# Kernel tuning notes

Hardware: AMD Instinct MI355X
Metric: run time of the kernel (lower is better)

The kernel has to match this reference:

```python
import jax, jax.numpy as jnp
import numpy as np

NUM_SAMPLES = 2048
MAX_AGENTS = 64
D_MODEL = 128
NUM_HEADS = 8


def setup_inputs() -> dict:
    key = jax.random.key(0)
    # deterministic ragged sizes: 1..64 repeating -> total = 32 * (64*65/2) = 66560
    agents = ((np.arange(NUM_SAMPLES) % MAX_AGENTS) + 1).astype(np.int32)
    total = int(agents.sum())
    k1, k2, k3 = jax.random.split(key, 3)
    s = 1.0 / np.sqrt(D_MODEL)
    return {
        "att_in": jax.random.normal(k1, (total, D_MODEL), jnp.float32),
        "in_proj_w": jax.random.uniform(k2, (3 * D_MODEL, D_MODEL), jnp.float32, -s, s),
        "in_proj_b": jnp.zeros((3 * D_MODEL,), jnp.float32),
        "out_proj_w": jax.random.uniform(k3, (D_MODEL, D_MODEL), jnp.float32, -s, s),
        "out_proj_b": jnp.zeros((D_MODEL,), jnp.float32),
        "agents_per_sample": jnp.asarray(agents),
    }


def reference(att_in, in_proj_w, in_proj_b, out_proj_w, out_proj_b, agents_per_sample):
    # agents_per_sample is static ragged metadata (host ints)
    agents = np.asarray(agents_per_sample)
    B = len(agents)
    A = int(agents.max())
    D = att_in.shape[-1]
    hd = D // NUM_HEADS

    # scatter ragged tokens into zero-padded [B, A, D]
    sample_ids = np.repeat(np.arange(B), agents)
    pos = np.concatenate([np.arange(n) for n in agents])
    padded = jnp.zeros((B, A, D), att_in.dtype).at[sample_ids, pos].set(att_in)
    key_valid = jnp.asarray(np.arange(A)[None, :] < agents[:, None])  # [B, A]

    # torch nn.MultiheadAttention math (eval mode, dropout=0)
    qkv = padded @ in_proj_w.T + in_proj_b  # [B, A, 3D]
    q, k, v = jnp.split(qkv, 3, axis=-1)
    q = q.reshape(B, A, NUM_HEADS, hd)
    k = k.reshape(B, A, NUM_HEADS, hd)
    v = v.reshape(B, A, NUM_HEADS, hd)

    scores = jnp.einsum("bqhd,bkhd->bhqk", q, k) / jnp.sqrt(jnp.asarray(hd, q.dtype))
    scores = jnp.where(key_valid[:, None, None, :], scores, jnp.asarray(-1e30, scores.dtype))
    attn = jax.nn.softmax(scores, axis=-1)

    out = jnp.einsum("bhqk,bkhd->bqhd", attn, v).reshape(B, A, D)
    out = out @ out_proj_w.T + out_proj_b

    # unpad: concatenation of the per-sample ragged outputs
    return out[sample_ids, pos]
```

## Files before the change

kernel.cpp:

```cpp
#include <hip/hip_runtime.h>

#define DM 128

typedef __attribute__((ext_vector_type(8))) __bf16 bf16x8;
typedef __attribute__((ext_vector_type(4))) float f32x4;

__device__ inline unsigned short f2bf(float f) {
    unsigned u = __float_as_uint(f);
    u += 0x7FFFu + ((u >> 16) & 1u);
    return (unsigned short)(u >> 16);
}

__global__ void prep(const int* __restrict__ agents, int B, int M,
                     const float* __restrict__ wqkv, const float* __restrict__ wout,
                     const float* __restrict__ x,
                     int* __restrict__ offs,
                     unsigned short* __restrict__ wqkv_bf,
                     unsigned short* __restrict__ wout_bf,
                     unsigned short* __restrict__ xbf) {
    if (blockIdx.x < 64) {
        int idx = (blockIdx.x * 256 + threadIdx.x) * 4;
        if (idx < 49152) {
            float4 v = *(const float4*)(wqkv + idx);
            ushort4 o;
            o.x = f2bf(v.x); o.y = f2bf(v.y); o.z = f2bf(v.z); o.w = f2bf(v.w);
            *(ushort4*)(wqkv_bf + idx) = o;
        } else {
            int j = idx - 49152;
            float4 v = *(const float4*)(wout + j);
            ushort4 o;
            o.x = f2bf(v.x); o.y = f2bf(v.y); o.z = f2bf(v.z); o.w = f2bf(v.w);
            *(ushort4*)(wout_bf + j) = o;
        }
    } else if (blockIdx.x == 64) {
        __shared__ int part[256];
        const int tid = threadIdx.x;
        const int per = (B + 255) >> 8;
        const int base = tid * per;
        int s = 0;
        for (int i = 0; i < per; ++i) {
            int idx = base + i;
            if (idx < B) s += agents[idx];
        }
        part[tid] = s;
        __syncthreads();
        for (int off = 1; off < 256; off <<= 1) {
            int v = (tid >= off) ? part[tid - off] : 0;
            __syncthreads();
            part[tid] += v;
            __syncthreads();
        }
        int run = (tid == 0) ? 0 : part[tid - 1];
        for (int i = 0; i < per; ++i) {
            int idx = base + i;
            if (idx < B) { offs[idx] = run; run += agents[idx]; }
        }
    } else {
        const int nf4 = M * 32;
        const int stride = ((int)gridDim.x - 65) * 256;
        for (int idx = ((int)blockIdx.x - 65) * 256 + (int)threadIdx.x; idx < nf4;
             idx += stride) {
            float4 v = ((const float4*)x)[idx];
            ushort4 o;
            o.x = f2bf(v.x); o.y = f2bf(v.y); o.z = f2bf(v.z); o.w = f2bf(v.w);
            ((ushort4*)xbf)[idx] = o;
        }
    }
}

template<int NT>
__device__ __forceinline__ void qa_body(
    const unsigned short* __restrict__ xbf,
    const unsigned short* __restrict__ wqkvb,
    const float* __restrict__ bqkv,
    unsigned short* __restrict__ obuf,
    int n, int base, int M, int h, int quad, int l16)
{
    constexpr int G   = (NT + 1) / 2;
    constexpr int KT2 = 2 * G;
    bf16x8 qf[NT], kf[NT], vA[G];
    #pragma unroll
    for (int g = 0; g < G; ++g) vA[g] = (bf16x8)(__bf16)0.0f;

    bf16x8 wfq[4], wfk[4], wfv[4];
    const unsigned short* wq = wqkvb + (size_t)(h * 16 + l16) * 128;
    #pragma unroll
    for (int ks = 0; ks < 4; ++ks) {
        wfq[ks] = *(const bf16x8*)(wq + ks * 32 + quad * 8);
        wfk[ks] = *(const bf16x8*)(wq + 128 * 128 + ks * 32 + quad * 8);
        wfv[ks] = *(const bf16x8*)(wq + 256 * 128 + ks * 32 + quad * 8);
    }
    const float4 bq4 = *(const float4*)(bqkv + h * 16 + quad * 4);
    const float4 bk4 = *(const float4*)(bqkv + 128 + h * 16 + quad * 4);
    const float  bv  = bqkv[256 + h * 16 + l16];

    const int shA = (quad & 1) * 32 + l16;
    const int shB = shA + 16;

    #pragma unroll
    for (int mt = 0; mt < NT; ++mt) {
        int row = base + mt * 16 + l16;
        row = row < M ? row : M - 1;
        const unsigned short* xr = xbf + (size_t)row * 128;
        bf16x8 xf[4];
        #pragma unroll
        for (int ks = 0; ks < 4; ++ks)
            xf[ks] = *(const bf16x8*)(xr + ks * 32 + quad * 8);
        f32x4 qa = {0.f,0.f,0.f,0.f}, ka = {0.f,0.f,0.f,0.f}, va = {0.f,0.f,0.f,0.f};
        #pragma unroll
        for (int ks = 0; ks < 4; ++ks) {
            qa = __builtin_amdgcn_mfma_f32_16x16x32_bf16(wfq[ks], xf[ks], qa, 0, 0, 0);
            ka = __builtin_amdgcn_mfma_f32_16x16x32_bf16(wfk[ks], xf[ks], ka, 0, 0, 0);
            va = __builtin_amdgcn_mfma_f32_16x16x32_bf16(xf[ks], wfv[ks], va, 0, 0, 0);
        }
        {
            ushort4 w;
            w.x = f2bf(qa[0] + bq4.x); w.y = f2bf(qa[1] + bq4.y);
            w.z = f2bf(qa[2] + bq4.z); w.w = f2bf(qa[3] + bq4.w);
            unsigned u0 = (unsigned)w.x | ((unsigned)w.y << 16);
            unsigned u1 = (unsigned)w.z | ((unsigned)w.w << 16);
            uint4 q;
            q.x = __shfl(u0, shA); q.y = __shfl(u1, shA);
            q.z = __shfl(u0, shB); q.w = __shfl(u1, shB);
            qf[mt] = (quad < 2) ? __builtin_bit_cast(bf16x8, q) : (bf16x8)(__bf16)0.0f;
        }
        {
            ushort4 w;
            w.x = f2bf(ka[0] + bk4.x); w.y = f2bf(ka[1] + bk4.y);
            w.z = f2bf(ka[2] + bk4.z); w.w = f2bf(ka[3] + bk4.w);
            unsigned u0 = (unsigned)w.x | ((unsigned)w.y << 16);
            unsigned u1 = (unsigned)w.z | ((unsigned)w.w << 16);
            uint4 q;
            q.x = __shfl(u0, shA); q.y = __shfl(u1, shA);
            q.z = __shfl(u0, shB); q.w = __shfl(u1, shB);
            kf[mt] = (quad < 2) ? __builtin_bit_cast(bf16x8, q) : (bf16x8)(__bf16)0.0f;
        }
        #pragma unroll
        for (int r = 0; r < 4; ++r)
            vA[mt >> 1][(mt & 1) * 4 + r] = (__bf16)(va[r] + bv);
    }

    int thr[KT2];
    #pragma unroll
    for (int kt = 0; kt < KT2; ++kt) {
        int t = n - kt * 16 - quad * 4;
        thr[kt] = t < 0 ? 0 : (t > 4 ? 4 : t);
    }
    const float SC2 = 0.25f * 1.44269504088896340736f;

    #pragma unroll
    for (int mt = 0; mt < NT; ++mt) {
        float pr[KT2][4];
        float mm = -3.0e38f;
        #pragma unroll
        for (int kt = 0; kt < KT2; ++kt) {
            if (kt < NT) {
                f32x4 sc = __builtin_amdgcn_mfma_f32_16x16x32_bf16(
                    kf[kt], qf[mt], (f32x4){0.f, 0.f, 0.f, 0.f}, 0, 0, 0);
                #pragma unroll
                for (int r = 0; r < 4; ++r) {
                    float v = sc[r] * SC2;
                    pr[kt][r] = v;
                    mm = fmaxf(mm, v);
                }
            } else {
                #pragma unroll
                for (int r = 0; r < 4; ++r) pr[kt][r] = -3.0e38f;
            }
        }
        mm = fmaxf(mm, __shfl_xor(mm, 16));
        mm = fmaxf(mm, __shfl_xor(mm, 32));
        float ll = 0.f;
        #pragma unroll
        for (int kt = 0; kt < KT2; ++kt)
            #pragma unroll
            for (int r = 0; r < 4; ++r) {
                float e = exp2f(pr[kt][r] - mm);
                e = (r < thr[kt]) ? e : 0.f;
                pr[kt][r] = e;
                ll += e;
            }
        ll += __shfl_xor(ll, 16);
        ll += __shfl_xor(ll, 32);
        float inv = __builtin_amdgcn_rcpf(ll);
        bf16x8 pf[G];
        #pragma unroll
        for (int g = 0; g < G; ++g)
            #pragma unroll
            for (int j = 0; j < 8; ++j)
                pf[g][j] = (__bf16)(pr[2 * g + (j >> 2)][j & 3] * inv);
        f32x4 o = __builtin_amdgcn_mfma_f32_16x16x32_bf16(
            vA[0], pf[0], (f32x4){0.f, 0.f, 0.f, 0.f}, 0, 0, 0);
        if constexpr (G == 2)
            o = __builtin_amdgcn_mfma_f32_16x16x32_bf16(vA[1], pf[1], o, 0, 0, 0);
        const int row = mt * 16 + l16;
        if (row < n) {
            ushort4 w;
            w.x = f2bf(o[0]); w.y = f2bf(o[1]); w.z = f2bf(o[2]); w.w = f2bf(o[3]);
            *(ushort4*)(obuf + (size_t)(base + row) * 256 + h * 16 + quad * 4) = w;
        }
    }
}

__launch_bounds__(64, 3)
__global__ void qkvattn(const unsigned short* __restrict__ xbf,
                        const unsigned short* __restrict__ wqkvb,
                        const float* __restrict__ bqkv,
                        unsigned short* __restrict__ obuf,
                        const int* __restrict__ agents,
                        const int* __restrict__ offs,
                        int M) {
    const int bid = blockIdx.x;
    const int s = bid >> 3, h = bid & 7;
    const int n = agents[s];
    const int base = offs[s];
    const int lane = threadIdx.x & 63, quad = lane >> 4, l16 = lane & 15;
    const int nt = (n + 15) >> 4;
    if      (nt == 1) qa_body<1>(xbf, wqkvb, bqkv, obuf, n, base, M, h, quad, l16);
    else if (nt == 2) qa_body<2>(xbf, wqkvb, bqkv, obuf, n, base, M, h, quad, l16);
    else if (nt == 3) qa_body<3>(xbf, wqkvb, bqkv, obuf, n, base, M, h, quad, l16);
    else              qa_body<4>(xbf, wqkvb, bqkv, obuf, n, base, M, h, quad, l16);
}

__launch_bounds__(256, 4)
__global__ void oproj(const unsigned short* __restrict__ attn_b,
                      const unsigned short* __restrict__ woutb,
                      const float* __restrict__ bout,
                      float* __restrict__ out, int M) {
    __shared__ __align__(16) unsigned short Ws[128 * 136];
    __shared__ __align__(16) float biass[128];
    const int m0 = blockIdx.x * 64;
    const int tid = threadIdx.x;

    for (int f = tid; f < 2048; f += 256) {
        int t = f >> 4, c = f & 15;
        *(uint4*)&Ws[t * 136 + c * 8] = *(const uint4*)(woutb + (size_t)t * 128 + c * 8);
    }
    if (tid < 32)
        ((float4*)biass)[tid] = ((const float4*)bout)[tid];
    __syncthreads();

    const int wave = tid >> 6, lane = tid & 63, quad = lane >> 4, l16 = lane & 15;
    const int mw = m0 + wave * 16;

    bf16x8 af[4];
    {
        int row = mw + l16;
        row = (row < M) ? row : (M - 1);
        #pragma unroll
        for (int ks = 0; ks < 4; ++ks)
            af[ks] = *(const bf16x8*)(attn_b + (size_t)row * 256 + ks * 32 + quad * 8);
    }

    const int row0 = mw + l16;

    for (int ct = 0; ct < 8; ++ct) {
        bf16x8 bc[4];
        #pragma unroll
        for (int ks = 0; ks < 4; ++ks)
            bc[ks] = *(const bf16x8*)&Ws[(ct * 16 + l16) * 136 + ks * 32 + quad * 8];
        f32x4 a0 = {0.f, 0.f, 0.f, 0.f};
        #pragma unroll
        for (int ks = 0; ks < 4; ++ks)
            a0 = __builtin_amdgcn_mfma_f32_16x16x32_bf16(bc[ks], af[ks], a0, 0, 0, 0);
        const int n0 = ct * 16 + quad * 4;
        const float4 b4 = *(const float4*)(biass + n0);
        float4 o0;
        o0.x = a0[0] + b4.x; o0.y = a0[1] + b4.y; o0.z = a0[2] + b4.z; o0.w = a0[3] + b4.w;
        if (row0 < M) *(float4*)(out + (size_t)row0 * DM + n0) = o0;
    }
}

extern "C" void kernel_launch(void* const* d_in, const int* in_sizes, int n_in,
                              void* d_out, int out_size, void* d_ws, size_t ws_size,
                              hipStream_t stream) {
    const float* att_in     = (const float*)d_in[0];
    const float* in_proj_w  = (const float*)d_in[1];
    const float* in_proj_b  = (const float*)d_in[2];
    const float* out_proj_w = (const float*)d_in[3];
    const float* out_proj_b = (const float*)d_in[4];
    const int*   agents     = (const int*)d_in[5];
    const int B = in_sizes[5];
    const int M = out_size / DM;

    int* offs = (int*)d_ws;
    unsigned short* wqkv_bf = (unsigned short*)((char*)d_ws + 8192);
    unsigned short* wout_bf = (unsigned short*)((char*)d_ws + 106496);
    unsigned short* xbf     = (unsigned short*)((char*)d_ws + 139264);
    unsigned short* obuf    = (unsigned short*)d_out;

    hipLaunchKernelGGL(prep, dim3(65 + 1024), dim3(256), 0, stream,
                       agents, B, M, in_proj_w, out_proj_w, att_in,
                       offs, wqkv_bf, wout_bf, xbf);
    hipLaunchKernelGGL(qkvattn, dim3(B * 8), dim3(64), 0, stream,
                       xbf, wqkv_bf, in_proj_b, obuf, agents, offs, M);
    hipLaunchKernelGGL(oproj, dim3((M + 63) / 64), dim3(256), 0, stream,
                       obuf, wout_bf, out_proj_b, (float*)d_out, M);
}
```

Baseline: 153.2 us.

## Process two heads per wavefront in fused QKV-attention kernel to reuse x tiles

Each 64-thread block now handles two attention heads instead of one, halving the grid size. The input x fragments are loaded once and reused for both heads' Q/K/V MFMA projections, which cuts redundant global loads of x and gives the MFMA pipe more independent work to interleave. The cost is roughly double the register footprint for weights and the Q/K/V fragments, so launch bounds drop from 3 to 2 waves per SIMD. Fewer, larger blocks may also reduce parallelism.

Result: no change. 154.8 us (+1.0%).

```diff
diff --git a/kernel.cpp b/kernel.cpp
--- a/kernel.cpp
+++ b/kernel.cpp
@@ -74,25 +74,33 @@
     const unsigned short* __restrict__ wqkvb,
     const float* __restrict__ bqkv,
     unsigned short* __restrict__ obuf,
-    int n, int base, int M, int h, int quad, int l16)
+    int n, int base, int M, int hp, int quad, int l16)
 {
     constexpr int G   = (NT + 1) / 2;
     constexpr int KT2 = 2 * G;
-    bf16x8 qf[NT], kf[NT], vA[G];
-    #pragma unroll
-    for (int g = 0; g < G; ++g) vA[g] = (bf16x8)(__bf16)0.0f;
-
-    bf16x8 wfq[4], wfk[4], wfv[4];
-    const unsigned short* wq = wqkvb + (size_t)(h * 16 + l16) * 128;
-    #pragma unroll
-    for (int ks = 0; ks < 4; ++ks) {
-        wfq[ks] = *(const bf16x8*)(wq + ks * 32 + quad * 8);
-        wfk[ks] = *(const bf16x8*)(wq + 128 * 128 + ks * 32 + quad * 8);
-        wfv[ks] = *(const bf16x8*)(wq + 256 * 128 + ks * 32 + quad * 8);
-    }
-    const float4 bq4 = *(const float4*)(bqkv + h * 16 + quad * 4);
-    const float4 bk4 = *(const float4*)(bqkv + 128 + h * 16 + quad * 4);
-    const float  bv  = bqkv[256 + h * 16 + l16];
+    bf16x8 qf[2][NT], kf[2][NT], vA[2][G];
+    #pragma unroll
+    for (int p = 0; p < 2; ++p)
+        #pragma unroll
+        for (int g = 0; g < G; ++g) vA[p][g] = (bf16x8)(__bf16)0.0f;
+
+    bf16x8 wfq[2][4], wfk[2][4], wfv[2][4];
+    float4 bq4[2], bk4[2];
+    float  bv[2];
+    #pragma unroll
+    for (int p = 0; p < 2; ++p) {
+        const int h = hp * 2 + p;
+        const unsigned short* wq = wqkvb + (size_t)(h * 16 + l16) * 128;
+        #pragma unroll
+        for (int ks = 0; ks < 4; ++ks) {
+            wfq[p][ks] = *(const bf16x8*)(wq + ks * 32 + quad * 8);
+            wfk[p][ks] = *(const bf16x8*)(wq + 128 * 128 + ks * 32 + quad * 8);
+            wfv[p][ks] = *(const bf16x8*)(wq + 256 * 128 + ks * 32 + quad * 8);
+        }
+        bq4[p] = *(const float4*)(bqkv + h * 16 + quad * 4);
+        bk4[p] = *(const float4*)(bqkv + 128 + h * 16 + quad * 4);
+        bv[p]  = bqkv[256 + h * 16 + l16];
+    }
 
     const int shA = (quad & 1) * 32 + l16;
     const int shB = shA + 16;
@@ -106,38 +114,49 @@
         #pragma unroll
         for (int ks = 0; ks < 4; ++ks)
             xf[ks] = *(const bf16x8*)(xr + ks * 32 + quad * 8);
-        f32x4 qa = {0.f,0.f,0.f,0.f}, ka = {0.f,0.f,0.f,0.f}, va = {0.f,0.f,0.f,0.f};
-        #pragma unroll
-        for (int ks = 0; ks < 4; ++ks) {
-            qa = __builtin_amdgcn_mfma_f32_16x16x32_bf16(wfq[ks], xf[ks], qa, 0, 0, 0);
-            ka = __builtin_amdgcn_mfma_f32_16x16x32_bf16(wfk[ks], xf[ks], ka, 0, 0, 0);
-            va = __builtin_amdgcn_mfma_f32_16x16x32_bf16(xf[ks], wfv[ks], va, 0, 0, 0);
-        }
-        {
-            ushort4 w;
-            w.x = f2bf(qa[0] + bq4.x); w.y = f2bf(qa[1] + bq4.y);
-            w.z = f2bf(qa[2] + bq4.z); w.w = f2bf(qa[3] + bq4.w);
-            unsigned u0 = (unsigned)w.x | ((unsigned)w.y << 16);
-            unsigned u1 = (unsigned)w.z | ((unsigned)w.w << 16);
-            uint4 q;
-            q.x = __shfl(u0, shA); q.y = __shfl(u1, shA);
-            q.z = __shfl(u0, shB); q.w = __shfl(u1, shB);
-            qf[mt] = (quad < 2) ? __builtin_bit_cast(bf16x8, q) : (bf16x8)(__bf16)0.0f;
-        }
-        {
-            ushort4 w;
-            w.x = f2bf(ka[0] + bk4.x); w.y = f2bf(ka[1] + bk4.y);
-            w.z = f2bf(ka[2] + bk4.z); w.w = f2bf(ka[3] + bk4.w);
-            unsigned u0 = (unsigned)w.x | ((unsigned)w.y << 16);
-            unsigned u1 = (unsigned)w.z | ((unsigned)w.w << 16);
-            uint4 q;
-            q.x = __shfl(u0, shA); q.y = __shfl(u1, shA);
-            q.z = __shfl(u0, shB); q.w = __shfl(u1, shB);
-            kf[mt] = (quad < 2) ? __builtin_bit_cast(bf16x8, q) : (bf16x8)(__bf16)0.0f;
-        }
-        #pragma unroll
-        for (int r = 0; r < 4; ++r)
-            vA[mt >> 1][(mt & 1) * 4 + r] = (__bf16)(va[r] + bv);
+        f32x4 qa[2], ka[2], va[2];
+        #pragma unroll
+        for (int p = 0; p < 2; ++p) {
+            qa[p] = (f32x4){0.f,0.f,0.f,0.f};
+            ka[p] = (f32x4){0.f,0.f,0.f,0.f};
+            va[p] = (f32x4){0.f,0.f,0.f,0.f};
+        }
+        #pragma unroll
+        for (int ks = 0; ks < 4; ++ks)
+            #pragma unroll
+            for (int p = 0; p < 2; ++p) {
+                qa[p] = __builtin_amdgcn_mfma_f32_16x16x32_bf16(wfq[p][ks], xf[ks], qa[p], 0, 0, 0);
+                ka[p] = __builtin_amdgcn_mfma_f32_16x16x32_bf16(wfk[p][ks], xf[ks], ka[p], 0, 0, 0);
+                va[p] = __builtin_amdgcn_mfma_f32_16x16x32_bf16(xf[ks], wfv[p][ks], va[p], 0, 0, 0);
+            }
+        #pragma unroll
+        for (int p = 0; p < 2; ++p) {
+            {
+                ushort4 w;
+                w.x = f2bf(qa[p][0] + bq4[p].x); w.y = f2bf(qa[p][1] + bq4[p].y);
+                w.z = f2bf(qa[p][2] + bq4[p].z); w.w = f2bf(qa[p][3] + bq4[p].w);
+                unsigned u0 = (unsigned)w.x | ((unsigned)w.y << 16);
+                unsigned u1 = (unsigned)w.z | ((unsigned)w.w << 16);
+                uint4 q;
+                q.x = __shfl(u0, shA); q.y = __shfl(u1, shA);
+                q.z = __shfl(u0, shB); q.w = __shfl(u1, shB);
+                qf[p][mt] = (quad < 2) ? __builtin_bit_cast(bf16x8, q) : (bf16x8)(__bf16)0.0f;
+            }
+            {
+                ushort4 w;
+                w.x = f2bf(ka[p][0] + bk4[p].x); w.y = f2bf(ka[p][1] + bk4[p].y);
+                w.z = f2bf(ka[p][2] + bk4[p].z); w.w = f2bf(ka[p][3] + bk4[p].w);
+                unsigned u0 = (unsigned)w.x | ((unsigned)w.y << 16);
+                unsigned u1 = (unsigned)w.z | ((unsigned)w.w << 16);
+                uint4 q;
+                q.x = __shfl(u0, shA); q.y = __shfl(u1, shA);
+                q.z = __shfl(u0, shB); q.w = __shfl(u1, shB);
+                kf[p][mt] = (quad < 2) ? __builtin_bit_cast(bf16x8, q) : (bf16x8)(__bf16)0.0f;
+            }
+            #pragma unroll
+            for (int r = 0; r < 4; ++r)
+                vA[p][mt >> 1][(mt & 1) * 4 + r] = (__bf16)(va[p][r] + bv[p]);
+        }
     }
 
     int thr[KT2];
@@ -149,60 +168,64 @@
     const float SC2 = 0.25f * 1.44269504088896340736f;
 
     #pragma unroll
-    for (int mt = 0; mt < NT; ++mt) {
-        float pr[KT2][4];
-        float mm = -3.0e38f;
-        #pragma unroll
-        for (int kt = 0; kt < KT2; ++kt) {
-            if (kt < NT) {
-                f32x4 sc = __builtin_amdgcn_mfma_f32_16x16x32_bf16(
-                    kf[kt], qf[mt], (f32x4){0.f, 0.f, 0.f, 0.f}, 0, 0, 0);
+    for (int p = 0; p < 2; ++p) {
+        const int ocol = (hp * 2 + p) * 16 + quad * 4;
+        #pragma unroll
+        for (int mt = 0; mt < NT; ++mt) {
+            float pr[KT2][4];
+            float mm = -3.0e38f;
+            #pragma unroll
+            for (int kt = 0; kt < KT2; ++kt) {
+                if (kt < NT) {
+                    f32x4 sc = __builtin_amdgcn_mfma_f32_16x16x32_bf16(
+                        kf[p][kt], qf[p][mt], (f32x4){0.f, 0.f, 0.f, 0.f}, 0, 0, 0);
+                    #pragma unroll
+                    for (int r = 0; r < 4; ++r) {
+                        float v = sc[r] * SC2;
+                        pr[kt][r] = v;
+                        mm = fmaxf(mm, v);
+                    }
+                } else {
+                    #pragma unroll
+                    for (int r = 0; r < 4; ++r) pr[kt][r] = -3.0e38f;
+                }
+            }
+            mm = fmaxf(mm, __shfl_xor(mm, 16));
+            mm = fmaxf(mm, __shfl_xor(mm, 32));
+            float ll = 0.f;
+            #pragma unroll
+            for (int kt = 0; kt < KT2; ++kt)
                 #pragma unroll
                 for (int r = 0; r < 4; ++r) {
-                    float v = sc[r] * SC2;
-                    pr[kt][r] = v;
-                    mm = fmaxf(mm, v);
+                    float e = exp2f(pr[kt][r] - mm);
+                    e = (r < thr[kt]) ? e : 0.f;
+                    pr[kt][r] = e;
+                    ll += e;
                 }
-            } else {
+            ll += __shfl_xor(ll, 16);
+            ll += __shfl_xor(ll, 32);
+            float inv = __builtin_amdgcn_rcpf(ll);
+            bf16x8 pf[G];
+            #pragma unroll
+            for (int g = 0; g < G; ++g)
                 #pragma unroll
-                for (int r = 0; r < 4; ++r) pr[kt][r] = -3.0e38f;
-            }
-        }
-        mm = fmaxf(mm, __shfl_xor(mm, 16));
-        mm = fmaxf(mm, __shfl_xor(mm, 32));
-        float ll = 0.f;
-        #pragma unroll
-        for (int kt = 0; kt < KT2; ++kt)
-            #pragma unroll
-            for (int r = 0; r < 4; ++r) {
-                float e = exp2f(pr[kt][r] - mm);
-                e = (r < thr[kt]) ? e : 0.f;
-                pr[kt][r] = e;
-                ll += e;
-            }
-        ll += __shfl_xor(ll, 16);
-        ll += __shfl_xor(ll, 32);
-        float inv = __builtin_amdgcn_rcpf(ll);
-        bf16x8 pf[G];
-        #pragma unroll
-        for (int g = 0; g < G; ++g)
-            #pragma unroll
-            for (int j = 0; j < 8; ++j)
-                pf[g][j] = (__bf16)(pr[2 * g + (j >> 2)][j & 3] * inv);
-        f32x4 o = __builtin_amdgcn_mfma_f32_16x16x32_bf16(
-            vA[0], pf[0], (f32x4){0.f, 0.f, 0.f, 0.f}, 0, 0, 0);
-        if constexpr (G == 2)
-            o = __builtin_amdgcn_mfma_f32_16x16x32_bf16(vA[1], pf[1], o, 0, 0, 0);
-        const int row = mt * 16 + l16;
-        if (row < n) {
-            ushort4 w;
-            w.x = f2bf(o[0]); w.y = f2bf(o[1]); w.z = f2bf(o[2]); w.w = f2bf(o[3]);
-            *(ushort4*)(obuf + (size_t)(base + row) * 256 + h * 16 + quad * 4) = w;
-        }
-    }
-}
-
-__launch_bounds__(64, 3)
+                for (int j = 0; j < 8; ++j)
+                    pf[g][j] = (__bf16)(pr[2 * g + (j >> 2)][j & 3] * inv);
+            f32x4 o = __builtin_amdgcn_mfma_f32_16x16x32_bf16(
+                vA[p][0], pf[0], (f32x4){0.f, 0.f, 0.f, 0.f}, 0, 0, 0);
+            if constexpr (G == 2)
+                o = __builtin_amdgcn_mfma_f32_16x16x32_bf16(vA[p][1], pf[1], o, 0, 0, 0);
+            const int row = mt * 16 + l16;
+            if (row < n) {
+                ushort4 w;
+                w.x = f2bf(o[0]); w.y = f2bf(o[1]); w.z = f2bf(o[2]); w.w = f2bf(o[3]);
+                *(ushort4*)(obuf + (size_t)(base + row) * 256 + ocol) = w;
+            }
+        }
+    }
+}
+
+__launch_bounds__(64, 2)
 __global__ void qkvattn(const unsigned short* __restrict__ xbf,
                         const unsigned short* __restrict__ wqkvb,
                         const float* __restrict__ bqkv,
@@ -211,15 +234,15 @@
                         const int* __restrict__ offs,
                         int M) {
     const int bid = blockIdx.x;
-    const int s = bid >> 3, h = bid & 7;
+    const int s = bid >> 2, hp = bid & 3;
     const int n = agents[s];
     const int base = offs[s];
     const int lane = threadIdx.x & 63, quad = lane >> 4, l16 = lane & 15;
     const int nt = (n + 15) >> 4;
-    if      (nt == 1) qa_body<1>(xbf, wqkvb, bqkv, obuf, n, base, M, h, quad, l16);
-    else if (nt == 2) qa_body<2>(xbf, wqkvb, bqkv, obuf, n, base, M, h, quad, l16);
-    else if (nt == 3) qa_body<3>(xbf, wqkvb, bqkv, obuf, n, base, M, h, quad, l16);
-    else              qa_body<4>(xbf, wqkvb, bqkv, obuf, n, base, M, h, quad, l16);
+    if      (nt == 1) qa_body<1>(xbf, wqkvb, bqkv, obuf, n, base, M, hp, quad, l16);
+    else if (nt == 2) qa_body<2>(xbf, wqkvb, bqkv, obuf, n, base, M, hp, quad, l16);
+    else if (nt == 3) qa_body<3>(xbf, wqkvb, bqkv, obuf, n, base, M, hp, quad, l16);
+    else              qa_body<4>(xbf, wqkvb, bqkv, obuf, n, base, M, hp, quad, l16);
 }
 
 __launch_bounds__(256, 4)
@@ -292,7 +315,7 @@
     hipLaunchKernelGGL(prep, dim3(65 + 1024), dim3(256), 0, stream,
                        agents, B, M, in_proj_w, out_proj_w, att_in,
                        offs, wqkv_bf, wout_bf, xbf);
-    hipLaunchKernelGGL(qkvattn, dim3(B * 8), dim3(64), 0, stream,
+    hipLaunchKernelGGL(qkvattn, dim3(B * 4), dim3(64), 0, stream,
                        xbf, wqkv_bf, in_proj_b, obuf, agents, offs, M);
     hipLaunchKernelGGL(oproj, dim3((M + 63) / 64), dim3(256), 0, stream,
                        obuf, wout_bf, out_proj_b, (float*)d_out, M);
```
